# Performance work log

Hardware: AMD Instinct MI355X
Metric: run time of the kernel (lower is better)

## Reference

```python
import jax, jax.numpy as jnp
import numpy as np
from jax import lax

L, T, DM, DH = 4, 4096, 2048, 1024
MAX_PHASE = 6.28
EPS = 1e-5


def setup_inputs() -> dict:
    key = jax.random.key(0)
    ks = jax.random.split(key, 16)
    # LRU initializers (r_min=0, r_max=1)
    u1 = jax.random.uniform(ks[0], (L, DH))
    nu_log = jnp.log(-0.5 * jnp.log(u1))
    u2 = jax.random.uniform(ks[1], (L, DH))
    theta_log = jnp.log(MAX_PHASE * u2)
    abs_lam = jnp.exp(-jnp.exp(nu_log))  # |lambda|
    gamma_log = jnp.log(jnp.sqrt(1.0 - abs_lam ** 2))
    B_re = jax.random.normal(ks[2], (L, DH, DM)) / np.sqrt(2 * DM)
    B_im = jax.random.normal(ks[3], (L, DH, DM)) / np.sqrt(2 * DM)
    C_re = jax.random.normal(ks[4], (L, DM, DH)) / np.sqrt(DH)
    C_im = jax.random.normal(ks[5], (L, DM, DH)) / np.sqrt(DH)
    D = jax.random.normal(ks[6], (L, DM))
    bound = 1.0 / np.sqrt(DM)
    enc_w = jax.random.uniform(ks[7], (DM, DM), minval=-bound, maxval=bound)
    enc_b = jax.random.uniform(ks[8], (DM,), minval=-bound, maxval=bound)
    out1_w = jax.random.uniform(ks[9], (L, DM, DM), minval=-bound, maxval=bound)
    out1_b = jax.random.uniform(ks[10], (L, DM), minval=-bound, maxval=bound)
    out2_w = jax.random.uniform(ks[11], (L, DM, DM), minval=-bound, maxval=bound)
    out2_b = jax.random.uniform(ks[12], (L, DM), minval=-bound, maxval=bound)
    norm_w = jnp.ones((L, DM))
    norm_b = jnp.zeros((L, DM))
    x = jax.random.normal(ks[13], (T, DM))
    return dict(x=x, enc_w=enc_w, enc_b=enc_b, nu_log=nu_log, theta_log=theta_log,
                gamma_log=gamma_log, B_re=B_re, B_im=B_im, C_re=C_re, C_im=C_im,
                D=D, norm_w=norm_w, norm_b=norm_b, out1_w=out1_w, out1_b=out1_b,
                out2_w=out2_w, out2_b=out2_b)


def _lru(xn, nu, th, gl, br, bi, cr, ci, d):
    # xn: (T, DM) real -> (T, DM) real
    lam = jnp.exp(-jnp.exp(nu) + 1j * jnp.exp(th))          # (DH,) complex
    B_norm = (br + 1j * bi) * jnp.exp(gl)[:, None]           # (DH, DM)
    Bu = xn.astype(B_norm.dtype) @ B_norm.T                  # (T, DH) complex
    a = jnp.broadcast_to(lam, Bu.shape)
    def combine(e1, e2):
        a1, b1 = e1
        a2, b2 = e2
        return a1 * a2, a2 * b1 + b2
    _, h = lax.associative_scan(combine, (a, Bu), axis=0)    # h_t = lam*h_{t-1} + Bu_t
    C = cr + 1j * ci
    return (h @ C.T).real + xn * d


def _batchnorm(x, w, b):
    # training-mode BatchNorm1d over dim 0 (biased variance), matching torch
    mu = x.mean(axis=0)
    var = jnp.mean((x - mu) ** 2, axis=0)
    return (x - mu) / jnp.sqrt(var + EPS) * w + b


def _forward(x, enc_w, enc_b, nu_log, theta_log, gamma_log, B_re, B_im,
             C_re, C_im, D, norm_w, norm_b, out1_w, out1_b, out2_w, out2_b):
    x = x @ enc_w.T + enc_b
    def layer(carry, p):
        nu, th, gl, br, bi, cr, ci, d, nw, nb, w1, b1, w2, b2 = p
        xn = _batchnorm(carry, nw, nb)
        y = _lru(xn, nu, th, gl, br, bi, cr, ci, d)
        y = jax.nn.gelu(y, approximate=False)
        y = (y @ w1.T + b1) * jax.nn.sigmoid(y @ w2.T + b2)
        return carry + y, None
    x, _ = lax.scan(layer, x, (nu_log, theta_log, gamma_log, B_re, B_im,
                               C_re, C_im, D, norm_w, norm_b,
                               out1_w, out1_b, out2_w, out2_b))
    return x


def reference(x, enc_w, enc_b, nu_log, theta_log, gamma_log, B_re, B_im,
              C_re, C_im, D, norm_w, norm_b, out1_w, out1_b, out2_w, out2_b):
    return _forward(x, enc_w, enc_b, nu_log, theta_log, gamma_log, B_re, B_im,
                    C_re, C_im, D, norm_w, norm_b, out1_w, out1_b, out2_w, out2_b)
```

## Files before the change

### kernel.cpp

```cpp
#include <hip/hip_runtime.h>
#include <stdint.h>
#include <math.h>


#define LAYERS 4
#define TT     4096
#define DMODEL 2048
#define DHID   1024
#define NCHUNK 64
#define CLEN   64
#define KTILES 64

typedef unsigned short ushort_t;
typedef __attribute__((ext_vector_type(8))) _Float16 half8;
typedef __attribute__((ext_vector_type(4))) float    f32x4;

__device__ __forceinline__ unsigned pack2h(float a, float b) {
  _Float16 ha = (_Float16)a, hb = (_Float16)b;
  unsigned short ua = *(unsigned short*)&ha, ub = *(unsigned short*)&hb;
  return (unsigned)ua | ((unsigned)ub << 16);
}

__device__ __forceinline__ void get_lam(const float* nu_log, const float* th_log,
                                        int h, float& lre, float& lim)
{
  const float mag = expf(-expf(nu_log[h]));
  const float th  = expf(th_log[h]);
  lre = mag * cosf(th);
  lim = mag * sinf(th);
}

__global__ __launch_bounds__(256)
void convert_h(const float* __restrict__ B0, const float* __restrict__ B1,
               int ldb, int NS, int KS, ushort_t* __restrict__ Hi)
{
  __shared__ float tile[128][33];
  const int mb  = blockIdx.x;
  const int kb  = blockIdx.y;
  const int tid = threadIdx.x;
  const int r0  = tid >> 3;
  const int c0  = (tid & 7) * 4;
#pragma unroll
  for (int rep = 0; rep < 4; ++rep) {
    const int rr = rep * 32 + r0;
    const int n  = mb * 128 + rr;
    const int k  = kb * 32 + c0;
    const float* bp; long idx;
    if (n >= NS)      { bp = B1; idx = (long)(n - NS) * ldb + k; }
    else if (k >= KS) { bp = B1; idx = (long)n * ldb + (k - KS); }
    else              { bp = B0; idx = (long)n * ldb + k; }
#pragma unroll
    for (int u = 0; u < 4; ++u) tile[rr][c0 + u] = bp[idx + u];
  }
  __syncthreads();
#pragma unroll
  for (int rep = 0; rep < 2; ++rep) {
    const int id2 = rep * 256 + tid;
    const int kg  = id2 >> 7;
    const int m   = id2 & 127;
    const long off = ((long)mb * KTILES + kb) * 4096 + (kg * 128 + m) * 8;
    unsigned hw[4];
#pragma unroll
    for (int p = 0; p < 4; ++p)
      hw[p] = pack2h(tile[m][kg * 8 + p * 2], tile[m][kg * 8 + p * 2 + 1]);
    *(uint4*)&Hi[off] = make_uint4(hw[0], hw[1], hw[2], hw[3]);
  }
}

__global__ __launch_bounds__(256)
void convert_ilv_rows(const float* __restrict__ P0, const float* __restrict__ P1,
                      int ldb, ushort_t* __restrict__ Hi)
{
  __shared__ float tile[128][33];
  const int mb  = blockIdx.x;
  const int kb  = blockIdx.y;
  const int tid = threadIdx.x;
  const int r0  = tid >> 3;
  const int c0  = (tid & 7) * 4;
#pragma unroll
  for (int rep = 0; rep < 4; ++rep) {
    const int rr = rep * 32 + r0;
    const int n  = mb * 128 + rr;
    const float* bp = (n & 1) ? P1 : P0;
    const long idx = (long)(n >> 1) * ldb + kb * 32 + c0;
#pragma unroll
    for (int u = 0; u < 4; ++u) tile[rr][c0 + u] = bp[idx + u];
  }
  __syncthreads();
#pragma unroll
  for (int rep = 0; rep < 2; ++rep) {
    const int id2 = rep * 256 + tid;
    const int kg  = id2 >> 7;
    const int m   = id2 & 127;
    const long off = ((long)mb * KTILES + kb) * 4096 + (kg * 128 + m) * 8;
    unsigned hw[4];
#pragma unroll
    for (int p = 0; p < 4; ++p)
      hw[p] = pack2h(tile[m][kg * 8 + p * 2], tile[m][kg * 8 + p * 2 + 1]);
    *(uint4*)&Hi[off] = make_uint4(hw[0], hw[1], hw[2], hw[3]);
  }
}

__global__ __launch_bounds__(256)
void convert_ilv_cols(const float* __restrict__ P0, const float* __restrict__ P1,
                      int ldb, ushort_t* __restrict__ Hi)
{
  __shared__ float tile[128][33];
  const int mb  = blockIdx.x;
  const int kb  = blockIdx.y;
  const int tid = threadIdx.x;
  const int r0  = tid >> 3;
  const int c0  = (tid & 7) * 4;
#pragma unroll
  for (int rep = 0; rep < 4; ++rep) {
    const int rr = rep * 32 + r0;
    const int n  = mb * 128 + rr;
    const long base = (long)n * ldb + ((kb * 32 + c0) >> 1);
    tile[rr][c0 + 0] = P0[base];
    tile[rr][c0 + 1] = P1[base];
    tile[rr][c0 + 2] = P0[base + 1];
    tile[rr][c0 + 3] = P1[base + 1];
  }
  __syncthreads();
#pragma unroll
  for (int rep = 0; rep < 2; ++rep) {
    const int id2 = rep * 256 + tid;
    const int kg  = id2 >> 7;
    const int m   = id2 & 127;
    const long off = ((long)mb * KTILES + kb) * 4096 + (kg * 128 + m) * 8;
    unsigned hw[4];
#pragma unroll
    for (int p = 0; p < 4; ++p)
      hw[p] = pack2h(tile[m][kg * 8 + p * 2], tile[m][kg * 8 + p * 2 + 1]);
    *(uint4*)&Hi[off] = make_uint4(hw[0], hw[1], hw[2], hw[3]);
  }
}

__global__ __launch_bounds__(256)
void bn_convert(const float* __restrict__ carry, const float* __restrict__ stats,
                const float* __restrict__ nw, const float* __restrict__ nb,
                ushort_t* __restrict__ Hi)
{
  __shared__ float tile[128][33];
  const int mb  = blockIdx.x;
  const int kb  = blockIdx.y;
  const int tid = threadIdx.x;
  const int r0  = tid >> 3;
  const int c0  = (tid & 7) * 4;
  float mean[4], rstd[4], w_[4], b_[4];
#pragma unroll
  for (int u = 0; u < 4; ++u) {
    const int j = kb * 32 + c0 + u;
    const float mu = stats[j] * (1.0f / TT);
    const float va = fmaxf(stats[DMODEL + j] * (1.0f / TT) - mu * mu, 0.0f);
    mean[u] = mu; rstd[u] = rsqrtf(va + 1e-5f);
    w_[u] = nw[j]; b_[u] = nb[j];
  }
#pragma unroll
  for (int rep = 0; rep < 4; ++rep) {
    const int rr  = rep * 32 + r0;
    const long base = (long)(mb * 128 + rr) * 2048 + kb * 32 + c0;
#pragma unroll
    for (int u = 0; u < 4; ++u)
      tile[rr][c0 + u] = (carry[base + u] - mean[u]) * rstd[u] * w_[u] + b_[u];
  }
  __syncthreads();
#pragma unroll
  for (int rep = 0; rep < 2; ++rep) {
    const int id2 = rep * 256 + tid;
    const int kg  = id2 >> 7;
    const int m   = id2 & 127;
    const long off = ((long)mb * KTILES + kb) * 4096 + (kg * 128 + m) * 8;
    unsigned hw[4];
#pragma unroll
    for (int p = 0; p < 4; ++p)
      hw[p] = pack2h(tile[m][kg * 8 + p * 2], tile[m][kg * 8 + p * 2 + 1]);
    *(uint4*)&Hi[off] = make_uint4(hw[0], hw[1], hw[2], hw[3]);
  }
}

__global__ __launch_bounds__(256)
void scan3_convert(const float* __restrict__ loc,
                   const float* __restrict__ ccre, const float* __restrict__ ccim,
                   const float* __restrict__ nu_log, const float* __restrict__ th_log,
                   ushort_t* __restrict__ Hi)
{
  __shared__ float tile[128][33];
  const int mb  = blockIdx.x;
  const int kb  = blockIdx.y;
  const int tid = threadIdx.x;
  const int r0  = tid >> 3;
  const int c0  = (tid & 7) * 4;
  float en[4], eth[4], cr0[4], ci0[4], cr1[4], ci1[4];
  int   im[4];
#pragma unroll
  for (int u = 0; u < 4; ++u) {
    const int col = kb * 32 + c0 + u;
    const int h   = col >> 1;
    im[u]  = col & 1;
    en[u]  = expf(nu_log[h]);
    eth[u] = expf(th_log[h]);
    cr0[u] = ccre[(mb * 2) * DHID + h];     ci0[u] = ccim[(mb * 2) * DHID + h];
    cr1[u] = ccre[(mb * 2 + 1) * DHID + h]; ci1[u] = ccim[(mb * 2 + 1) * DHID + h];
  }
#pragma unroll
  for (int rep = 0; rep < 4; ++rep) {
    const int rr  = rep * 32 + r0;
    const int sel = rr >> 6;
    const float p = (float)((rr & 63) + 1);
    const long base = (long)(mb * 128 + rr) * 2048 + kb * 32 + c0;
#pragma unroll
    for (int u = 0; u < 4; ++u) {
      const float magp = expf(-p * en[u]);
      const float ang  = p * eth[u];
      float sv, cv;
      __sincosf(ang, &sv, &cv);
      const float pr = magp * cv, pi = magp * sv;
      const float cr_ = sel ? cr1[u] : cr0[u];
      const float ci_ = sel ? ci1[u] : ci0[u];
      const float L = loc[base + u];
      tile[rr][c0 + u] = im[u] ? -(L + pr * ci_ + pi * cr_)
                               :  (L + pr * cr_ - pi * ci_);
    }
  }
  __syncthreads();
#pragma unroll
  for (int rep = 0; rep < 2; ++rep) {
    const int id2 = rep * 256 + tid;
    const int kg  = id2 >> 7;
    const int m   = id2 & 127;
    const long off = ((long)mb * KTILES + kb) * 4096 + (kg * 128 + m) * 8;
    unsigned hw[4];
#pragma unroll
    for (int p2 = 0; p2 < 4; ++p2)
      hw[p2] = pack2h(tile[m][kg * 8 + p2 * 2], tile[m][kg * 8 + p2 * 2 + 1]);
    *(uint4*)&Hi[off] = make_uint4(hw[0], hw[1], hw[2], hw[3]);
  }
}

#define GLDS(gp, lp) __builtin_amdgcn_global_load_lds( \
    (__attribute__((address_space(1))) void*)(void*)(gp), \
    (__attribute__((address_space(3))) void*)(lp), 16, 0, 0)

__global__ __launch_bounds__(256)
void gemm_mfma(const ushort_t* __restrict__ Ahi, const ushort_t* __restrict__ Bhi,
               float* __restrict__ C, const float* __restrict__ bias,
               int epi, float* __restrict__ stats,
               ushort_t* __restrict__ gT,
               const float* __restrict__ dvec,
               const float* __restrict__ nu_log, const float* __restrict__ th_log,
               const float* __restrict__ gl_log)
{
  __shared__ ushort_t S[2][16384];
  const int tid  = threadIdx.x;
  const int lane = tid & 63;
  const int wid  = tid >> 6;
  const int wm   = wid >> 1;
  const int wn   = wid & 1;

  const int bid = blockIdx.y * gridDim.x + blockIdx.x;
  const int xcd = bid & 7, idx = bid >> 3;
  const int mb  = ((xcd & 3) << 3) | (idx & 7);
  const int nb  = ((xcd >> 2) << 3) | (idx >> 3);

  f32x4 acc[4][4];
#pragma unroll
  for (int i = 0; i < 4; ++i)
#pragma unroll
    for (int j = 0; j < 4; ++j) acc[i][j] = (f32x4){0.f, 0.f, 0.f, 0.f};

  const ushort_t* ga = Ahi + (long)mb * KTILES * 4096 + tid * 8;
  const ushort_t* gb = Bhi + (long)nb * KTILES * 4096 + tid * 8;

  const int albase = ((lane >> 4) * 128 + wm * 64 + (lane & 15)) * 8;
  const int blbase = ((lane >> 4) * 128 + wn * 64 + (lane & 15)) * 8;

  half8 A0[4], B0[4], A1[4], B1[4];

#define STAGE(P) \
  GLDS(ga,        &S[P][tid * 8]); \
  GLDS(ga + 2048, &S[P][2048 + tid * 8]); \
  GLDS(ga + 4096, &S[P][4096 + tid * 8]); \
  GLDS(ga + 6144, &S[P][6144 + tid * 8]); \
  GLDS(gb,        &S[P][8192 + tid * 8]); \
  GLDS(gb + 2048, &S[P][10240 + tid * 8]); \
  GLDS(gb + 4096, &S[P][12288 + tid * 8]); \
  GLDS(gb + 6144, &S[P][14336 + tid * 8]); \
  ga += 8192; gb += 8192;

#define RD(P) \
  _Pragma("unroll") \
  for (int m = 0; m < 4; ++m) A0[m] = *(const half8*)&S[P][albase + m * 128]; \
  _Pragma("unroll") \
  for (int n = 0; n < 4; ++n) B0[n] = *(const half8*)&S[P][8192 + blbase + n * 128]; \
  _Pragma("unroll") \
  for (int m = 0; m < 4; ++m) A1[m] = *(const half8*)&S[P][4096 + albase + m * 128]; \
  _Pragma("unroll") \
  for (int n = 0; n < 4; ++n) B1[n] = *(const half8*)&S[P][12288 + blbase + n * 128];

#define MFMA16(A_, B_) \
  _Pragma("unroll") \
  for (int m = 0; m < 4; ++m) \
    _Pragma("unroll") \
    for (int n = 0; n < 4; ++n) \
      acc[m][n] = __builtin_amdgcn_mfma_f32_16x16x32_f16(A_[m], B_[n], acc[m][n], 0, 0, 0);

#define WAIT_VM_BAR(n) asm volatile("s_waitcnt vmcnt(" #n ")" ::: "memory"); \
  __builtin_amdgcn_sched_barrier(0); __builtin_amdgcn_s_barrier();
#define LGKM0_BAR asm volatile("s_waitcnt lgkmcnt(0)" ::: "memory"); \
  __builtin_amdgcn_sched_barrier(0); __builtin_amdgcn_s_barrier();

#define KSTEP(P) \
  WAIT_VM_BAR(8) \
  RD(P) \
  __builtin_amdgcn_s_setprio(1); \
  MFMA16(A0, B0) \
  MFMA16(A1, B1) \
  __builtin_amdgcn_s_setprio(0); \
  LGKM0_BAR \
  STAGE(P)

  STAGE(0)
  STAGE(1)
  for (int it = 0; it < 15; ++it) {
    KSTEP(0)
    KSTEP(1)
  }
  WAIT_VM_BAR(8)
  RD(0)
  __builtin_amdgcn_s_setprio(1);
  MFMA16(A0, B0)
  MFMA16(A1, B1)
  __builtin_amdgcn_s_setprio(0);
  WAIT_VM_BAR(0)
  RD(1)
  __builtin_amdgcn_s_setprio(1);
  MFMA16(A0, B0)
  MFMA16(A1, B1)
  __builtin_amdgcn_s_setprio(0);
#undef STAGE
#undef RD
#undef MFMA16
#undef WAIT_VM_BAR
#undef LGKM0_BAR
#undef KSTEP

  const int cn = lane & 15;
  const int cr = (lane >> 4) * 4;

  if (epi == 0) {
    float s0[4] = {0.f, 0.f, 0.f, 0.f}, s1[4] = {0.f, 0.f, 0.f, 0.f};
#pragma unroll
    for (int m = 0; m < 4; ++m) {
      const long row = (long)mb * 128 + wm * 64 + m * 16 + cr;
#pragma unroll
      for (int n = 0; n < 4; ++n) {
        const int col = nb * 128 + wn * 64 + n * 16 + cn;
        const float bv = bias ? bias[col] : 0.0f;
#pragma unroll
        for (int q = 0; q < 4; ++q) {
          const float v = acc[m][n][q] + bv;
          C[(row + q) * 2048 + col] = v;
          s0[n] += v; s1[n] += v * v;
        }
      }
    }
    if (stats) {
      __syncthreads();
      float* sred = (float*)&S[0][0];
      if (tid < 256) sred[tid] = 0.f;
      __syncthreads();
#pragma unroll
      for (int n = 0; n < 4; ++n) {
        const int lc = wn * 64 + n * 16 + cn;
        atomicAdd(&sred[lc], s0[n]);
        atomicAdd(&sred[128 + lc], s1[n]);
      }
      __syncthreads();
      if (tid < 128) {
        atomicAdd(&stats[nb * 128 + tid], sred[tid]);
        atomicAdd(&stats[DMODEL + nb * 128 + tid], sred[128 + tid]);
      }
    }
    return;
  }

  __syncthreads();
  float* Lf = (float*)&S[0][0];
#pragma unroll
  for (int m = 0; m < 4; ++m) {
    const int r = wm * 64 + m * 16 + cr;
#pragma unroll
    for (int n = 0; n < 4; ++n) {
      const int c = wn * 64 + n * 16 + cn;
#pragma unroll
      for (int q = 0; q < 4; ++q)
        Lf[(r + q) * 128 + c] = acc[m][n][q];
    }
  }
  __syncthreads();

  if (epi == 1) {
    if (tid < 128) {
      const int p  = tid & 63;
      const int ch = tid >> 6;
      const int hg = nb * 64 + p;
      const float gamma = expf(gl_log[hg]);
      float lre, lim; get_lam(nu_log, th_log, hg, lre, lim);
      float hr = 0.f, hi = 0.f;
      const long base = ((long)mb * 128 + ch * 64) * 2048 + nb * 128 + 2 * p;
      for (int i = 0; i < 64; ++i) {
        const float br_ = Lf[(ch * 64 + i) * 128 + 2 * p]     * gamma;
        const float bi_ = Lf[(ch * 64 + i) * 128 + 2 * p + 1] * gamma;
        const float nr = lre * hr - lim * hi + br_;
        const float ni = lre * hi + lim * hr + bi_;
        hr = nr; hi = ni;
        *(float2*)&C[base + (long)i * 2048] = make_float2(hr, hi);
      }
    }
    return;
  }

  {
    const int cb = nb * 4;
#pragma unroll
    for (int c = 0; c < 8; ++c) {
      const int chunk = c * 256 + tid;
      const int m  = chunk & 127;
      const int kg = (chunk >> 7) & 3;
      const int lt = chunk >> 9;
      const long off = ((long)mb * KTILES + cb + lt) * 4096 + (kg * 128 + m) * 8;
      const half8 xh = *(const half8*)&gT[off];
      const float* Lrow = &Lf[m * 128 + lt * 32 + kg * 8];
      const float* dp = dvec + nb * 128 + lt * 32 + kg * 8;
      unsigned hw[4];
#pragma unroll
      for (int p = 0; p < 4; ++p) {
        float g2[2];
#pragma unroll
        for (int e = 0; e < 2; ++e) {
          const int j = p * 2 + e;
          const float v = Lrow[j] + (float)xh[j] * dp[j];
          g2[e] = 0.5f * v * (1.0f + erff(v * 0.70710678118654752440f));
        }
        hw[p] = pack2h(g2[0], g2[1]);
      }
      *(uint4*)&gT[off] = make_uint4(hw[0], hw[1], hw[2], hw[3]);
    }
  }
}

__global__ __launch_bounds__(256)
void gemm_dual(const ushort_t* __restrict__ Ahi, const ushort_t* __restrict__ B1t,
               const ushort_t* __restrict__ B2t,
               float* __restrict__ carry, const float* __restrict__ b1,
               const float* __restrict__ b2, float* __restrict__ stats)
{
  __shared__ ushort_t S[3][8192];
  const int tid  = threadIdx.x;
  const int lane = tid & 63;
  const int wid  = tid >> 6;
  const int wm   = wid >> 1;
  const int wn   = wid & 1;

  const int bid = blockIdx.y * gridDim.x + blockIdx.x;
  const int xcd = bid & 7, idx = bid >> 3;
  const int mb  = ((xcd & 3) << 3) | (idx & 7);
  const int nbb = ((xcd >> 2) << 4) | (idx >> 3);

  f32x4 acc1[4][2], acc2[4][2];
#pragma unroll
  for (int i = 0; i < 4; ++i)
#pragma unroll
    for (int j = 0; j < 2; ++j) {
      acc1[i][j] = (f32x4){0.f, 0.f, 0.f, 0.f};
      acc2[i][j] = (f32x4){0.f, 0.f, 0.f, 0.f};
    }

  const int nt = nbb >> 1;
  const int hb = nbb & 1;

  const ushort_t* ga = Ahi + (long)mb * KTILES * 4096 + tid * 8;
  const long boff = ((tid >> 6) * 128 + hb * 64 + (tid & 63)) * 8;
  const ushort_t* g1 = B1t + (long)nt * KTILES * 4096 + boff;
  const ushort_t* g2 = B2t + (long)nt * KTILES * 4096 + boff;

  const int albase = ((lane >> 4) * 128 + wm * 64 + (lane & 15)) * 8;
  const int blbase = ((lane >> 4) * 64 + wn * 32 + (lane & 15)) * 8;

  half8 Af[4], B1f[2], B2f[2];

#define STAGE(P) \
  GLDS(ga,        &S[P][tid * 8]); \
  GLDS(ga + 2048, &S[P][2048 + tid * 8]); \
  GLDS(g1,        &S[P][4096 + tid * 8]); \
  GLDS(g2,        &S[P][6144 + tid * 8]); \
  ga += 4096; g1 += 4096; g2 += 4096;

#define RD(P) \
  _Pragma("unroll") \
  for (int m = 0; m < 4; ++m) Af[m]  = *(const half8*)&S[P][albase + m * 128]; \
  _Pragma("unroll") \
  for (int n = 0; n < 2; ++n) B1f[n] = *(const half8*)&S[P][4096 + blbase + n * 128]; \
  _Pragma("unroll") \
  for (int n = 0; n < 2; ++n) B2f[n] = *(const half8*)&S[P][6144 + blbase + n * 128];

#define MFMA16D \
  __builtin_amdgcn_s_setprio(1); \
  _Pragma("unroll") \
  for (int m = 0; m < 4; ++m) \
    _Pragma("unroll") \
    for (int n = 0; n < 2; ++n) \
      acc1[m][n] = __builtin_amdgcn_mfma_f32_16x16x32_f16(Af[m], B1f[n], acc1[m][n], 0, 0, 0); \
  _Pragma("unroll") \
  for (int m = 0; m < 4; ++m) \
    _Pragma("unroll") \
    for (int n = 0; n < 2; ++n) \
      acc2[m][n] = __builtin_amdgcn_mfma_f32_16x16x32_f16(Af[m], B2f[n], acc2[m][n], 0, 0, 0); \
  __builtin_amdgcn_s_setprio(0);

#define WAITB(n) asm volatile("s_waitcnt vmcnt(" #n ") lgkmcnt(0)" ::: "memory"); \
  __builtin_amdgcn_sched_barrier(0); __builtin_amdgcn_s_barrier();

#define KSTEPD(PRD, PST) \
  WAITB(4) \
  STAGE(PST) \
  RD(PRD) \
  MFMA16D

  STAGE(0)
  STAGE(1)
  for (int it = 0; it < 20; ++it) {
    KSTEPD(0, 2)
    KSTEPD(1, 0)
    KSTEPD(2, 1)
  }
  KSTEPD(0, 2)
  KSTEPD(1, 0)
  WAITB(4)
  RD(2)
  MFMA16D
  WAITB(0)
  RD(0)
  MFMA16D
#undef STAGE
#undef RD
#undef MFMA16D
#undef WAITB
#undef KSTEPD

  const int cn = lane & 15;
  const int cr = (lane >> 4) * 4;
  float s0[2] = {0.f, 0.f}, s1[2] = {0.f, 0.f};
#pragma unroll
  for (int m = 0; m < 4; ++m) {
    const long row = (long)mb * 128 + wm * 64 + m * 16 + cr;
#pragma unroll
    for (int n = 0; n < 2; ++n) {
      const int col = nbb * 64 + wn * 32 + n * 16 + cn;
      const float b1v = b1[col], b2v = b2[col];
#pragma unroll
      for (int q = 0; q < 4; ++q) {
        const long idx2 = (row + q) * 2048 + col;
        const float t1v = acc1[m][n][q] + b1v;
        const float t2v = acc2[m][n][q] + b2v;
        const float v = carry[idx2] + t1v * (1.0f / (1.0f + expf(-t2v)));
        carry[idx2] = v;
        s0[n] += v; s1[n] += v * v;
      }
    }
  }
  if (stats) {
    __syncthreads();
    float* sred = (float*)&S[0][0];
    if (tid < 128) sred[tid] = 0.f;
    __syncthreads();
#pragma unroll
    for (int n = 0; n < 2; ++n) {
      const int lc = wn * 32 + n * 16 + cn;
      atomicAdd(&sred[lc], s0[n]);
      atomicAdd(&sred[64 + lc], s1[n]);
    }
    __syncthreads();
    if (tid < 64) {
      atomicAdd(&stats[nbb * 64 + tid], sred[tid]);
      atomicAdd(&stats[DMODEL + nbb * 64 + tid], sred[64 + tid]);
    }
  }
}

__global__ void scan2(const float* __restrict__ loc,
                      float* __restrict__ ccre, float* __restrict__ ccim,
                      const float* __restrict__ nu_log, const float* __restrict__ th_log)
{
  const int h = blockIdx.x * 256 + threadIdx.x;
  float lre, lim; get_lam(nu_log, th_log, h, lre, lim);
  float ar = lre, ai = lim;
  for (int s = 0; s < 6; ++s) { float nr = ar * ar - ai * ai, ni = 2.f * ar * ai; ar = nr; ai = ni; }
  float er = 0.f, ei = 0.f;
  for (int c = 0; c < NCHUNK; ++c) {
    ccre[c * DHID + h] = er; ccim[c * DHID + h] = ei;
    const long t = (long)c * CLEN + (CLEN - 1);
    const float nr = ar * er - ai * ei + loc[t * 2048 + 2 * h];
    const float ni = ar * ei + ai * er + loc[t * 2048 + 2 * h + 1];
    er = nr; ei = ni;
  }
}

__global__ void finalize(const float* __restrict__ carry, float* __restrict__ out)
{
  const long idx = (long)blockIdx.x * 256 + threadIdx.x;
  const float v = carry[idx];
  out[idx] = (v == v && fabsf(v) < 3.0e38f) ? v : 300000.0f;
}

__global__ void diagfill(float* __restrict__ out, float val)
{
  const long idx = (long)blockIdx.x * 256 + threadIdx.x;
  out[idx] = (idx == 0) ? val : 0.0f;
}

extern "C" void kernel_launch(void* const* d_in, const int* in_sizes, int n_in,
                              void* d_out, int out_size, void* d_ws, size_t ws_size,
                              hipStream_t stream)
{
  (void)out_size;
  const int EW = (TT * DMODEL) / 256;
  float* out = (float*)d_out;

  if (n_in != 17 || in_sizes[0] != TT * DMODEL) {
    diagfill<<<EW, 256, 0, stream>>>(out, (float)(1 << 18));
    return;
  }
  if (ws_size < 151600000ull) {
    diagfill<<<EW, 256, 0, stream>>>(out, (float)(1 << 12));
    return;
  }

  const float* x     = (const float*)d_in[0];
  const float* enc_w = (const float*)d_in[1];
  const float* enc_b = (const float*)d_in[2];
  const float* nu    = (const float*)d_in[3];
  const float* th    = (const float*)d_in[4];
  const float* gl    = (const float*)d_in[5];
  const float* Bre   = (const float*)d_in[6];
  const float* Bim   = (const float*)d_in[7];
  const float* Cre   = (const float*)d_in[8];
  const float* Cim   = (const float*)d_in[9];
  const float* Dd    = (const float*)d_in[10];
  const float* nw    = (const float*)d_in[11];
  const float* nb    = (const float*)d_in[12];
  const float* w1    = (const float*)d_in[13];
  const float* b1    = (const float*)d_in[14];
  const float* w2    = (const float*)d_in[15];
  const float* b2    = (const float*)d_in[16];

  char* ws = (char*)d_ws;
  float*    carry = (float*)(ws);
  ushort_t* AhiX  = (ushort_t*)(ws + 33554432);
  float*    buf1  = (float*)(ws + 67108864);
  ushort_t* Ahi   = (ushort_t*)(ws + 100663296);
  ushort_t* B2hi  = (ushort_t*)(ws + 117440512);
  ushort_t* Bhi   = (ushort_t*)(ws + 134217728);
  float*    ccre  = (float*)(ws + 150994944);
  float*    ccim  = (float*)(ws + 151257088);
  float*    stats = (float*)(ws + 151519232);

  const dim3 gcA(32, 64);
  const dim3 gcW(16, 64);
  const dim3 gg(32, 16);
  const dim3 gg2(32, 32);
  const int BIG = 1 << 30;

  hipMemsetAsync(stats, 0, 2 * DMODEL * sizeof(float), stream);
  convert_h<<<gcA, 256, 0, stream>>>(x, x, 2048, BIG, BIG, Ahi);
  convert_h<<<gcW, 256, 0, stream>>>(enc_w, enc_w, 2048, BIG, BIG, Bhi);
  gemm_mfma<<<gg, 256, 0, stream>>>(Ahi, Bhi, carry, enc_b, 0, stats,
                                    nullptr, nullptr, nullptr, nullptr, nullptr);

  for (int l = 0; l < LAYERS; ++l) {
    const float* Brl = Bre + (size_t)l * DHID * DMODEL;
    const float* Bil = Bim + (size_t)l * DHID * DMODEL;
    const float* Crl = Cre + (size_t)l * DMODEL * DHID;
    const float* Cil = Cim + (size_t)l * DMODEL * DHID;
    const float* w1l = w1 + (size_t)l * DMODEL * DMODEL;
    const float* w2l = w2 + (size_t)l * DMODEL * DMODEL;

    bn_convert<<<gcA, 256, 0, stream>>>(carry, stats, nw + l * DMODEL,
                                        nb + l * DMODEL, AhiX);

    convert_ilv_rows<<<gcW, 256, 0, stream>>>(Brl, Bil, 2048, Bhi);
    gemm_mfma<<<gg, 256, 0, stream>>>(AhiX, Bhi, buf1, nullptr, 1, nullptr,
                                      nullptr, nullptr,
                                      nu + l * DHID, th + l * DHID, gl + l * DHID);

    scan2<<<4, 256, 0, stream>>>(buf1, ccre, ccim, nu + l * DHID, th + l * DHID);

    convert_ilv_cols<<<gcW, 256, 0, stream>>>(Crl, Cil, 1024, Bhi);
    scan3_convert<<<gcA, 256, 0, stream>>>(buf1, ccre, ccim, nu + l * DHID,
                                           th + l * DHID, Ahi);

    gemm_mfma<<<gg, 256, 0, stream>>>(Ahi, Bhi, nullptr, nullptr, 2, nullptr,
                                      AhiX, Dd + l * DMODEL,
                                      nullptr, nullptr, nullptr);

    convert_h<<<gcW, 256, 0, stream>>>(w1l, w1l, 2048, BIG, BIG, Bhi);
    convert_h<<<gcW, 256, 0, stream>>>(w2l, w2l, 2048, BIG, BIG, B2hi);
    float* nstats = (l < LAYERS - 1) ? stats : nullptr;
    if (nstats) hipMemsetAsync(stats, 0, 2 * DMODEL * sizeof(float), stream);
    gemm_dual<<<gg2, 256, 0, stream>>>(AhiX, Bhi, B2hi, carry,
                                       b1 + l * DMODEL, b2 + l * DMODEL, nstats);
  }

  finalize<<<EW, 256, 0, stream>>>(carry, out);
}
```

Before: 1.231 ms.

## Halve GEMM LDS footprint and raise occupancy with K=32 stages and split epilogue

The main MFMA GEMM now stages one 32-wide K slice per buffer instead of two, halving shared memory and halving the A/B fragment registers. The epilogues are reworked to dump accumulators to LDS in two 64-row halves so the smaller buffer suffices. The dual GEMM drops from triple to double buffering with a wait-then-restage ordering. Both kernels get launch_bounds(256,4) to allow more resident blocks per CU. The cost is twice as many barriers and K-loop iterations, less prefetch depth in the dual GEMM, and extra syncs in the epilogues.

```diff
diff --git a/kernel.cpp b/kernel.cpp
--- a/kernel.cpp
+++ b/kernel.cpp
@@ -242,7 +242,7 @@
     (__attribute__((address_space(1))) void*)(void*)(gp), \
     (__attribute__((address_space(3))) void*)(lp), 16, 0, 0)
 
-__global__ __launch_bounds__(256)
+__global__ __launch_bounds__(256, 4)
 void gemm_mfma(const ushort_t* __restrict__ Ahi, const ushort_t* __restrict__ Bhi,
                float* __restrict__ C, const float* __restrict__ bias,
                int epi, float* __restrict__ stats,
@@ -251,7 +251,7 @@
                const float* __restrict__ nu_log, const float* __restrict__ th_log,
                const float* __restrict__ gl_log)
 {
-  __shared__ ushort_t S[2][16384];
+  __shared__ ushort_t S[2][8192];
   const int tid  = threadIdx.x;
   const int lane = tid & 63;
   const int wid  = tid >> 6;
@@ -275,35 +275,29 @@
   const int albase = ((lane >> 4) * 128 + wm * 64 + (lane & 15)) * 8;
   const int blbase = ((lane >> 4) * 128 + wn * 64 + (lane & 15)) * 8;
 
-  half8 A0[4], B0[4], A1[4], B1[4];
+  half8 Af[4], Bf[4];
 
 #define STAGE(P) \
   GLDS(ga,        &S[P][tid * 8]); \
   GLDS(ga + 2048, &S[P][2048 + tid * 8]); \
-  GLDS(ga + 4096, &S[P][4096 + tid * 8]); \
-  GLDS(ga + 6144, &S[P][6144 + tid * 8]); \
-  GLDS(gb,        &S[P][8192 + tid * 8]); \
-  GLDS(gb + 2048, &S[P][10240 + tid * 8]); \
-  GLDS(gb + 4096, &S[P][12288 + tid * 8]); \
-  GLDS(gb + 6144, &S[P][14336 + tid * 8]); \
-  ga += 8192; gb += 8192;
+  GLDS(gb,        &S[P][4096 + tid * 8]); \
+  GLDS(gb + 2048, &S[P][6144 + tid * 8]); \
+  ga += 4096; gb += 4096;
 
 #define RD(P) \
   _Pragma("unroll") \
-  for (int m = 0; m < 4; ++m) A0[m] = *(const half8*)&S[P][albase + m * 128]; \
+  for (int m = 0; m < 4; ++m) Af[m] = *(const half8*)&S[P][albase + m * 128]; \
   _Pragma("unroll") \
-  for (int n = 0; n < 4; ++n) B0[n] = *(const half8*)&S[P][8192 + blbase + n * 128]; \
-  _Pragma("unroll") \
-  for (int m = 0; m < 4; ++m) A1[m] = *(const half8*)&S[P][4096 + albase + m * 128]; \
-  _Pragma("unroll") \
-  for (int n = 0; n < 4; ++n) B1[n] = *(const half8*)&S[P][12288 + blbase + n * 128];
-
-#define MFMA16(A_, B_) \
+  for (int n = 0; n < 4; ++n) Bf[n] = *(const half8*)&S[P][4096 + blbase + n * 128];
+
+#define MFMA16 \
+  __builtin_amdgcn_s_setprio(1); \
   _Pragma("unroll") \
   for (int m = 0; m < 4; ++m) \
     _Pragma("unroll") \
     for (int n = 0; n < 4; ++n) \
-      acc[m][n] = __builtin_amdgcn_mfma_f32_16x16x32_f16(A_[m], B_[n], acc[m][n], 0, 0, 0);
+      acc[m][n] = __builtin_amdgcn_mfma_f32_16x16x32_f16(Af[m], Bf[n], acc[m][n], 0, 0, 0); \
+  __builtin_amdgcn_s_setprio(0);
 
 #define WAIT_VM_BAR(n) asm volatile("s_waitcnt vmcnt(" #n ")" ::: "memory"); \
   __builtin_amdgcn_sched_barrier(0); __builtin_amdgcn_s_barrier();
@@ -311,33 +305,24 @@
   __builtin_amdgcn_sched_barrier(0); __builtin_amdgcn_s_barrier();
 
 #define KSTEP(P) \
-  WAIT_VM_BAR(8) \
+  WAIT_VM_BAR(4) \
   RD(P) \
-  __builtin_amdgcn_s_setprio(1); \
-  MFMA16(A0, B0) \
-  MFMA16(A1, B1) \
-  __builtin_amdgcn_s_setprio(0); \
+  MFMA16 \
   LGKM0_BAR \
   STAGE(P)
 
   STAGE(0)
   STAGE(1)
-  for (int it = 0; it < 15; ++it) {
+  for (int it = 0; it < 31; ++it) {
     KSTEP(0)
     KSTEP(1)
   }
-  WAIT_VM_BAR(8)
+  WAIT_VM_BAR(4)
   RD(0)
-  __builtin_amdgcn_s_setprio(1);
-  MFMA16(A0, B0)
-  MFMA16(A1, B1)
-  __builtin_amdgcn_s_setprio(0);
+  MFMA16
   WAIT_VM_BAR(0)
   RD(1)
-  __builtin_amdgcn_s_setprio(1);
-  MFMA16(A0, B0)
-  MFMA16(A1, B1)
-  __builtin_amdgcn_s_setprio(0);
+  MFMA16
 #undef STAGE
 #undef RD
 #undef MFMA16
@@ -385,78 +370,95 @@
     return;
   }
 
-  __syncthreads();
   float* Lf = (float*)&S[0][0];
-#pragma unroll
-  for (int m = 0; m < 4; ++m) {
-    const int r = wm * 64 + m * 16 + cr;
-#pragma unroll
-    for (int n = 0; n < 4; ++n) {
-      const int c = wn * 64 + n * 16 + cn;
-#pragma unroll
-      for (int q = 0; q < 4; ++q)
-        Lf[(r + q) * 128 + c] = acc[m][n][q];
-    }
-  }
-  __syncthreads();
 
   if (epi == 1) {
-    if (tid < 128) {
-      const int p  = tid & 63;
-      const int ch = tid >> 6;
-      const int hg = nb * 64 + p;
-      const float gamma = expf(gl_log[hg]);
-      float lre, lim; get_lam(nu_log, th_log, hg, lre, lim);
-      float hr = 0.f, hi = 0.f;
-      const long base = ((long)mb * 128 + ch * 64) * 2048 + nb * 128 + 2 * p;
-      for (int i = 0; i < 64; ++i) {
-        const float br_ = Lf[(ch * 64 + i) * 128 + 2 * p]     * gamma;
-        const float bi_ = Lf[(ch * 64 + i) * 128 + 2 * p + 1] * gamma;
-        const float nr = lre * hr - lim * hi + br_;
-        const float ni = lre * hi + lim * hr + bi_;
-        hr = nr; hi = ni;
-        *(float2*)&C[base + (long)i * 2048] = make_float2(hr, hi);
+    float gamma = 0.f, lre = 0.f, lim = 0.f;
+    if (tid < 64) {
+      const int hg = nb * 64 + tid;
+      gamma = expf(gl_log[hg]);
+      get_lam(nu_log, th_log, hg, lre, lim);
+    }
+#pragma unroll
+    for (int half = 0; half < 2; ++half) {
+      __syncthreads();
+      if (wm == half) {
+#pragma unroll
+        for (int m = 0; m < 4; ++m)
+#pragma unroll
+          for (int n = 0; n < 4; ++n)
+#pragma unroll
+            for (int q = 0; q < 4; ++q)
+              Lf[(m * 16 + cr + q) * 128 + wn * 64 + n * 16 + cn] = acc[m][n][q];
       }
+      __syncthreads();
+      if (tid < 64) {
+        const int p = tid;
+        float hr = 0.f, hi = 0.f;
+        const long base = ((long)mb * 128 + half * 64) * 2048 + nb * 128 + 2 * p;
+        for (int i = 0; i < 64; ++i) {
+          const float br_ = Lf[i * 128 + 2 * p]     * gamma;
+          const float bi_ = Lf[i * 128 + 2 * p + 1] * gamma;
+          const float nr = lre * hr - lim * hi + br_;
+          const float ni = lre * hi + lim * hr + bi_;
+          hr = nr; hi = ni;
+          *(float2*)&C[base + (long)i * 2048] = make_float2(hr, hi);
+        }
+      }
     }
     return;
   }
 
   {
-    const int cb = nb * 4;
-#pragma unroll
-    for (int c = 0; c < 8; ++c) {
-      const int chunk = c * 256 + tid;
-      const int m  = chunk & 127;
-      const int kg = (chunk >> 7) & 3;
-      const int lt = chunk >> 9;
-      const long off = ((long)mb * KTILES + cb + lt) * 4096 + (kg * 128 + m) * 8;
-      const half8 xh = *(const half8*)&gT[off];
-      const float* Lrow = &Lf[m * 128 + lt * 32 + kg * 8];
-      const float* dp = dvec + nb * 128 + lt * 32 + kg * 8;
-      unsigned hw[4];
-#pragma unroll
-      for (int p = 0; p < 4; ++p) {
-        float g2[2];
-#pragma unroll
-        for (int e = 0; e < 2; ++e) {
-          const int j = p * 2 + e;
-          const float v = Lrow[j] + (float)xh[j] * dp[j];
-          g2[e] = 0.5f * v * (1.0f + erff(v * 0.70710678118654752440f));
+#pragma unroll
+    for (int half = 0; half < 2; ++half) {
+      __syncthreads();
+      if (wm == half) {
+#pragma unroll
+        for (int m = 0; m < 4; ++m)
+#pragma unroll
+          for (int n = 0; n < 4; ++n)
+#pragma unroll
+            for (int q = 0; q < 4; ++q)
+              Lf[(m * 16 + cr + q) * 128 + wn * 64 + n * 16 + cn] = acc[m][n][q];
+      }
+      __syncthreads();
+#pragma unroll
+      for (int c = 0; c < 4; ++c) {
+        const int chunk = c * 256 + tid;
+        const int mloc = chunk & 63;
+        const int kg   = (chunk >> 6) & 3;
+        const int lt   = chunk >> 8;
+        const int m    = half * 64 + mloc;
+        const long off = ((long)mb * KTILES + nb * 4 + lt) * 4096 + (kg * 128 + m) * 8;
+        const half8 xh = *(const half8*)&gT[off];
+        const float* Lrow = &Lf[mloc * 128 + lt * 32 + kg * 8];
+        const float* dp = dvec + nb * 128 + lt * 32 + kg * 8;
+        unsigned hw[4];
+#pragma unroll
+        for (int p = 0; p < 4; ++p) {
+          float g2[2];
+#pragma unroll
+          for (int e = 0; e < 2; ++e) {
+            const int j = p * 2 + e;
+            const float v = Lrow[j] + (float)xh[j] * dp[j];
+            g2[e] = 0.5f * v * (1.0f + erff(v * 0.70710678118654752440f));
+          }
+          hw[p] = pack2h(g2[0], g2[1]);
         }
-        hw[p] = pack2h(g2[0], g2[1]);
+        *(uint4*)&gT[off] = make_uint4(hw[0], hw[1], hw[2], hw[3]);
       }
-      *(uint4*)&gT[off] = make_uint4(hw[0], hw[1], hw[2], hw[3]);
-    }
-  }
-}
-
-__global__ __launch_bounds__(256)
+    }
+  }
+}
+
+__global__ __launch_bounds__(256, 4)
 void gemm_dual(const ushort_t* __restrict__ Ahi, const ushort_t* __restrict__ B1t,
                const ushort_t* __restrict__ B2t,
                float* __restrict__ carry, const float* __restrict__ b1,
                const float* __restrict__ b2, float* __restrict__ stats)
 {
-  __shared__ ushort_t S[3][8192];
+  __shared__ ushort_t S[2][8192];
   const int tid  = threadIdx.x;
   const int lane = tid & 63;
   const int wid  = tid >> 6;
@@ -519,34 +521,35 @@
       acc2[m][n] = __builtin_amdgcn_mfma_f32_16x16x32_f16(Af[m], B2f[n], acc2[m][n], 0, 0, 0); \
   __builtin_amdgcn_s_setprio(0);
 
-#define WAITB(n) asm volatile("s_waitcnt vmcnt(" #n ") lgkmcnt(0)" ::: "memory"); \
+#define WAIT_VM_BAR(n) asm volatile("s_waitcnt vmcnt(" #n ")" ::: "memory"); \
   __builtin_amdgcn_sched_barrier(0); __builtin_amdgcn_s_barrier();
-
-#define KSTEPD(PRD, PST) \
-  WAITB(4) \
-  STAGE(PST) \
-  RD(PRD) \
-  MFMA16D
+#define LGKM0_BAR asm volatile("s_waitcnt lgkmcnt(0)" ::: "memory"); \
+  __builtin_amdgcn_sched_barrier(0); __builtin_amdgcn_s_barrier();
+
+#define KSTEPD(P) \
+  WAIT_VM_BAR(4) \
+  RD(P) \
+  MFMA16D \
+  LGKM0_BAR \
+  STAGE(P)
 
   STAGE(0)
   STAGE(1)
-  for (int it = 0; it < 20; ++it) {
-    KSTEPD(0, 2)
-    KSTEPD(1, 0)
-    KSTEPD(2, 1)
-  }
-  KSTEPD(0, 2)
-  KSTEPD(1, 0)
-  WAITB(4)
-  RD(2)
+  for (int it = 0; it < 31; ++it) {
+    KSTEPD(0)
+    KSTEPD(1)
+  }
+  WAIT_VM_BAR(4)
+  RD(0)
   MFMA16D
-  WAITB(0)
-  RD(0)
+  WAIT_VM_BAR(0)
+  RD(1)
   MFMA16D
 #undef STAGE
 #undef RD
 #undef MFMA16D
-#undef WAITB
+#undef WAIT_VM_BAR
+#undef LGKM0_BAR
 #undef KSTEPD
 
   const int cn = lane & 15;
```

New measurement: 1.178 ms. -4.3%, faster.
